# Kernel optimization log

Hardware: AMD Instinct MI355X
Metric: run time of the kernel (lower is better)

## Reference

```python
import jax, jax.numpy as jnp
import numpy as np

B, P, N, C = 8, 4, 512, 768
H = 12
HD = C // H  # 64
SCALE = HD ** -0.5


def setup_inputs() -> dict:
    key = jax.random.key(0)
    k1, k2, k3 = jax.random.split(key, 3)
    x = jax.random.normal(k1, (B, P, N, C), dtype=jnp.float32)
    W_qkv = jax.random.normal(k2, (3 * C, C), dtype=jnp.float32) * (C ** -0.5)
    W_proj = jax.random.normal(k3, (C, C), dtype=jnp.float32) * (C ** -0.5)
    b_proj = jnp.zeros((C,), dtype=jnp.float32)
    return {"x": x, "W_qkv": W_qkv, "W_proj": W_proj, "b_proj": b_proj}


def reference(x, W_qkv, W_proj, b_proj):
    b, p, n, c = x.shape
    # qkv projection (no bias): (B,P,N,3C) -> (B,P,N,3,H,HD)
    qkv = jnp.einsum('bpnc,dc->bpnd', x, W_qkv).reshape(b, p, n, 3, H, HD)
    # -> (3, B, P, H, N, HD)
    qkv = jnp.transpose(qkv, (3, 0, 1, 4, 2, 5))
    q, k, v = qkv[0], qkv[1], qkv[2]
    # scaled dot-product attention per (batch, patch, head)
    attn = jnp.einsum('bphnd,bphmd->bphnm', q * SCALE, k)
    attn = jax.nn.softmax(attn, axis=-1)
    out = jnp.einsum('bphnm,bphmd->bphnd', attn, v)
    # merge heads: (B,P,N,H,HD) -> (B,P,N,C)
    out = jnp.transpose(out, (0, 1, 3, 2, 4)).reshape(b, p, n, c)
    return jnp.einsum('bpnc,dc->bpnd', out, W_proj) + b_proj
```

## Files before the change

kernel.cpp:

```cpp
#include <hip/hip_runtime.h>

typedef _Float16 f16x8 __attribute__((ext_vector_type(8)));
typedef _Float16 f16x4 __attribute__((ext_vector_type(4)));
typedef unsigned short u16x8 __attribute__((ext_vector_type(8)));
typedef unsigned short u16x4 __attribute__((ext_vector_type(4)));
typedef float f32x4 __attribute__((ext_vector_type(4)));

#define GLOAD_LDS16(GP, LP)                                                        \
  __builtin_amdgcn_global_load_lds((const __attribute__((address_space(1))) void*)(GP), \
                                   (__attribute__((address_space(3))) void*)(LP), 16, 0, 0)

__device__ __forceinline__ unsigned int pkh(float a, float b) {
  return __builtin_bit_cast(unsigned int, __builtin_amdgcn_cvt_pkrtz(a, b));
}
__device__ __forceinline__ f16x8 ldfragh(const unsigned short* p) {
  return __builtin_bit_cast(f16x8, *(const u16x8*)p);
}
__device__ __forceinline__ f16x4 ldfragh4(const unsigned short* p) {
  return __builtin_bit_cast(f16x4, *(const u16x4*)p);
}
__device__ __forceinline__ f32x4 mfma32h(f16x8 a, f16x8 b, f32x4 c) {
  return __builtin_amdgcn_mfma_f32_16x16x32_f16(a, b, c, 0, 0, 0);
}
__device__ __forceinline__ f32x4 mfma16h(f16x4 a, f16x4 b, f32x4 c) {
  return __builtin_amdgcn_mfma_f32_16x16x16f16(a, b, c, 0, 0, 0);
}

#define MTOK   16384
#define CDIM   768
#define C3     2304
#define C2     1536
#define NX     12582912
#define NQW    1769472
#define NPW    589824

#define QSCALE_LOG2E 0.1803368801111204f

#define XB_OFF    0ul
#define WQKV_OFF  25165824ul
#define WPROJ_OFF 28704768ul
#define QK_OFF    29884416ul
#define VT_OFF    80216064ul

__global__ __launch_bounds__(256) void convert_kernel(
    const float* __restrict__ x, const float* __restrict__ wqkv,
    const float* __restrict__ wproj, unsigned short* __restrict__ xb,
    unsigned short* __restrict__ wqkvb, unsigned short* __restrict__ wprojb) {
  const int NX4 = NX / 4, NQ4 = NQW / 4, NP4 = NPW / 4;
  const int total = NX4 + NQ4 + NP4;
  for (int i = blockIdx.x * 256 + threadIdx.x; i < total; i += gridDim.x * 256) {
    const float4* src; unsigned short* dst; float scale = 1.f; int j;
    if (i < NX4) { src = (const float4*)x; dst = xb; j = i; }
    else if (i < NX4 + NQ4) {
      j = i - NX4; src = (const float4*)wqkv; dst = wqkvb;
      int d = (j * 4) / CDIM; if (d < CDIM) scale = QSCALE_LOG2E;
    } else { j = i - NX4 - NQ4; src = (const float4*)wproj; dst = wprojb; }
    float4 v = src[j];
    uint2 pk; pk.x = pkh(v.x * scale, v.y * scale); pk.y = pkh(v.z * scale, v.w * scale);
    *(uint2*)(dst + (long)j * 4) = pk;
  }
}

template <int MODE, int NCOLS>
__global__ __launch_bounds__(256) void gemm_bt(
    const unsigned short* __restrict__ A, const unsigned short* __restrict__ B,
    unsigned short* __restrict__ out_hf, unsigned short* __restrict__ out_vT,
    float* __restrict__ out_f32, const float* __restrict__ bias) {
  constexpr int K = 768;
  constexpr int NT = K / 64;
  __shared__ unsigned short As[2][128 * 64];
  __shared__ unsigned short Bs[2][128 * 64];
  const int tid = threadIdx.x;
  const int wave = tid >> 6, lane = tid & 63;
  const int wy = wave >> 1, wx = wave & 1;
  const int l15 = lane & 15, quad = lane >> 4;

  const int gid = blockIdx.x;
  const int g = gid >> 3;
  const int bm = ((g / NCOLS) << 3) + (gid & 7);
  const int bn = g % NCOLS;
  const bool swap = (MODE == 2) || (bn < 12);

  f32x4 acc[4][4];
  for (int i = 0; i < 4; i++)
    for (int j = 0; j < 4; j++) acc[i][j] = f32x4{0.f, 0.f, 0.f, 0.f};

  const unsigned short* Ab = A + (long)bm * 128 * K;
  const unsigned short* Bb = B + (long)bn * 128 * K;

  long goff[4]; int ldsoff[4];
  for (int i = 0; i < 4; i++) {
    int c = wave * 256 + i * 64 + lane;
    int row = c >> 3, q = c & 7;
    int srcq = q ^ (row & 7);
    goff[i] = (long)row * K + srcq * 8;
    ldsoff[i] = c * 8;
  }
  const int slot0 = (quad ^ (l15 & 7)) * 8;
  const int slot1 = ((4 + quad) ^ (l15 & 7)) * 8;

  for (int i = 0; i < 4; i++) {
    GLOAD_LDS16(Ab + goff[i], &As[0][ldsoff[i]]);
    GLOAD_LDS16(Bb + goff[i], &Bs[0][ldsoff[i]]);
  }

  for (int t = 0; t < NT; t++) {
    __syncthreads();
    if (t + 1 < NT) {
      const long kk = (long)(t + 1) * 64;
      const int nb = (t + 1) & 1;
      for (int i = 0; i < 4; i++) {
        GLOAD_LDS16(Ab + goff[i] + kk, &As[nb][ldsoff[i]]);
        GLOAD_LDS16(Bb + goff[i] + kk, &Bs[nb][ldsoff[i]]);
      }
    }
    const unsigned short* Ac = As[t & 1];
    const unsigned short* Bc = Bs[t & 1];
    for (int ks = 0; ks < 2; ks++) {
      const int sl = ks ? slot1 : slot0;
      f16x8 af[4], bfr[4];
      for (int mt = 0; mt < 4; mt++) af[mt]  = ldfragh(Ac + (wy * 64 + mt * 16 + l15) * 64 + sl);
      for (int nt = 0; nt < 4; nt++) bfr[nt] = ldfragh(Bc + (wx * 64 + nt * 16 + l15) * 64 + sl);
      if (swap) {
        for (int mt = 0; mt < 4; mt++)
          for (int nt = 0; nt < 4; nt++)
            acc[mt][nt] = mfma32h(bfr[nt], af[mt], acc[mt][nt]);
      } else {
        for (int mt = 0; mt < 4; mt++)
          for (int nt = 0; nt < 4; nt++)
            acc[mt][nt] = mfma32h(af[mt], bfr[nt], acc[mt][nt]);
      }
    }
  }

  if (MODE == 0) {
    if (bn < 12) {
      for (int mt = 0; mt < 4; mt++) {
        int m = bm * 128 + wy * 64 + mt * 16 + l15;
        for (int nt = 0; nt < 4; nt++) {
          int d0 = bn * 128 + wx * 64 + nt * 16 + quad * 4;
          uint2 pk; pk.x = pkh(acc[mt][nt][0], acc[mt][nt][1]);
          pk.y = pkh(acc[mt][nt][2], acc[mt][nt][3]);
          *(uint2*)(out_hf + (long)m * C2 + d0) = pk;
        }
      }
    } else {
      for (int mt = 0; mt < 4; mt++) {
        int mg = bm * 128 + wy * 64 + mt * 16 + quad * 4;
        int bp = mg >> 9, n0 = mg & 511;
        for (int nt = 0; nt < 4; nt++) {
          int dp = bn * 128 - C2 + wx * 64 + nt * 16 + l15;
          int hh = dp >> 6, e = dp & 63;
          uint2 pk; pk.x = pkh(acc[mt][nt][0], acc[mt][nt][1]);
          pk.y = pkh(acc[mt][nt][2], acc[mt][nt][3]);
          *(uint2*)(out_vT + ((long)((bp * 12 + hh) * 64 + e) * 512 + n0)) = pk;
        }
      }
    }
  } else {
    for (int nt = 0; nt < 4; nt++) {
      int d0 = bn * 128 + wx * 64 + nt * 16 + quad * 4;
      float4 bv = *(const float4*)(bias + d0);
      for (int mt = 0; mt < 4; mt++) {
        int m = bm * 128 + wy * 64 + mt * 16 + l15;
        float4 o;
        o.x = acc[mt][nt][0] + bv.x; o.y = acc[mt][nt][1] + bv.y;
        o.z = acc[mt][nt][2] + bv.z; o.w = acc[mt][nt][3] + bv.w;
        *(float4*)(out_f32 + (long)m * CDIM + d0) = o;
      }
    }
  }
}

__global__ __launch_bounds__(256, 4) void attn_kernel(
    const unsigned short* __restrict__ qk, const unsigned short* __restrict__ vT,
    unsigned short* __restrict__ aout) {
  const int bph = blockIdx.x;
  const int qt  = blockIdx.y;
  const int bp = bph / 12, h = bph % 12;
  const int tid = threadIdx.x;
  const int wave = tid >> 6, lane = tid & 63;
  const int l15 = lane & 15, quad = lane >> 4;

  __shared__ unsigned short Qs[128 * 72];
  __shared__ unsigned short Ks[64 * 72];
  __shared__ unsigned short Vs[64 * 72];

  const unsigned short* Qg = qk + (long)(bp * 512 + qt * 128) * C2 + h * 64;
  const unsigned short* Kg = qk + (long)(bp * 512) * C2 + CDIM + h * 64;
  const unsigned short* Vg = vT + (long)(bp * 12 + h) * 64 * 512;

  for (int i = 0; i < 4; i++) {
    int c = tid + i * 256;
    int row = c >> 3, c8 = c & 7;
    *(uint4*)(Qs + row * 72 + c8 * 8) = *(const uint4*)(Qg + (long)row * C2 + c8 * 8);
  }

  f32x4 o[2][4];
  float lrow[2] = {0.f, 0.f};
  for (int a = 0; a < 2; a++)
    for (int b = 0; b < 4; b++) o[a][b] = f32x4{0.f, 0.f, 0.f, 0.f};

  for (int ch = 0; ch < 8; ch++) {
    if (ch) __syncthreads();
    for (int i = 0; i < 2; i++) {
      int c = tid + i * 256;
      int row = c >> 3, c8 = c & 7;
      *(uint4*)(Ks + row * 72 + c8 * 8) = *(const uint4*)(Kg + (long)(ch * 64 + row) * C2 + c8 * 8);
      *(uint4*)(Vs + row * 72 + c8 * 8) = *(const uint4*)(Vg + (long)row * 512 + ch * 64 + c8 * 8);
    }
    __syncthreads();

    f32x4 st[2][4];
    for (int a = 0; a < 2; a++)
      for (int b = 0; b < 4; b++) st[a][b] = f32x4{0.f, 0.f, 0.f, 0.f};
    for (int ks = 0; ks < 2; ks++) {
      f16x8 qf[2];
      qf[0] = ldfragh(Qs + (wave * 32 +      l15) * 72 + ks * 32 + quad * 8);
      qf[1] = ldfragh(Qs + (wave * 32 + 16 + l15) * 72 + ks * 32 + quad * 8);
      for (int nt = 0; nt < 4; nt++) {
        f16x8 kf = ldfragh(Ks + (nt * 16 + l15) * 72 + ks * 32 + quad * 8);
        st[0][nt] = mfma32h(kf, qf[0], st[0][nt]);
        st[1][nt] = mfma32h(kf, qf[1], st[1][nt]);
      }
    }

    f16x4 pf[2][4];
    for (int mt2 = 0; mt2 < 2; mt2++) {
      float rs = 0.f;
      for (int nt = 0; nt < 4; nt++) {
        f32x4 p;
        for (int r = 0; r < 4; r++) {
          p[r] = __builtin_amdgcn_exp2f(st[mt2][nt][r]);
          rs += p[r];
        }
        uint2 pk2; pk2.x = pkh(p[0], p[1]); pk2.y = pkh(p[2], p[3]);
        pf[mt2][nt] = __builtin_bit_cast(f16x4, pk2);
      }
      lrow[mt2] += rs;
    }

    for (int nt = 0; nt < 4; nt++)
      for (int et = 0; et < 4; et++) {
        f16x4 vf = ldfragh4(Vs + (et * 16 + l15) * 72 + nt * 16 + quad * 4);
        o[0][et] = mfma16h(vf, pf[0][nt], o[0][et]);
        o[1][et] = mfma16h(vf, pf[1][nt], o[1][et]);
      }
  }

  for (int mt2 = 0; mt2 < 2; mt2++) {
    float l = lrow[mt2];
    l += __shfl_xor(l, 16);
    l += __shfl_xor(l, 32);
    float inv = 1.f / l;
    int q = qt * 128 + wave * 32 + mt2 * 16 + l15;
    for (int et = 0; et < 4; et++) {
      uint2 pk; pk.x = pkh(o[mt2][et][0] * inv, o[mt2][et][1] * inv);
      pk.y = pkh(o[mt2][et][2] * inv, o[mt2][et][3] * inv);
      *(uint2*)(aout + (long)(bp * 512 + q) * CDIM + h * 64 + et * 16 + quad * 4) = pk;
    }
  }
}

extern "C" void kernel_launch(void* const* d_in, const int* in_sizes, int n_in,
                              void* d_out, int out_size, void* d_ws, size_t ws_size,
                              hipStream_t stream) {
  (void)in_sizes; (void)n_in; (void)out_size; (void)ws_size;
  const float* x     = (const float*)d_in[0];
  const float* wqkv  = (const float*)d_in[1];
  const float* wproj = (const float*)d_in[2];
  const float* bproj = (const float*)d_in[3];
  float* out = (float*)d_out;
  char* ws = (char*)d_ws;

  unsigned short* xb     = (unsigned short*)(ws + XB_OFF);
  unsigned short* wqkvb  = (unsigned short*)(ws + WQKV_OFF);
  unsigned short* wprojb = (unsigned short*)(ws + WPROJ_OFF);
  unsigned short* qkbuf  = (unsigned short*)(ws + QK_OFF);
  unsigned short* vTbuf  = (unsigned short*)(ws + VT_OFF);
  unsigned short* attn_o = xb;

  convert_kernel<<<2048, 256, 0, stream>>>(x, wqkv, wproj, xb, wqkvb, wprojb);
  gemm_bt<0, 18><<<128 * 18, 256, 0, stream>>>(xb, wqkvb, qkbuf, vTbuf, nullptr, nullptr);
  attn_kernel<<<dim3(384, 4), 256, 0, stream>>>(qkbuf, vTbuf, attn_o);
  gemm_bt<2, 6><<<128 * 6, 256, 0, stream>>>(attn_o, wprojb, nullptr, nullptr, out, bproj);
}
```

Baseline: 268.5 us.

## Replace 128x128 GEMM with 256x256-tile, 8-wave, 4-stage pipelined GEMM

```diff
diff --git a/kernel.cpp b/kernel.cpp
--- a/kernel.cpp
+++ b/kernel.cpp
@@ -61,95 +61,130 @@
   }
 }
 
-template <int MODE, int NCOLS>
-__global__ __launch_bounds__(256) void gemm_bt(
+template <int MODE, int NTN>
+__global__ __launch_bounds__(512, 2) void gemm256(
     const unsigned short* __restrict__ A, const unsigned short* __restrict__ B,
     unsigned short* __restrict__ out_hf, unsigned short* __restrict__ out_vT,
     float* __restrict__ out_f32, const float* __restrict__ bias) {
   constexpr int K = 768;
-  constexpr int NT = K / 64;
-  __shared__ unsigned short As[2][128 * 64];
-  __shared__ unsigned short Bs[2][128 * 64];
+  constexpr int NKT = K / 32;
+  __shared__ unsigned short As[4][256 * 32];
+  __shared__ unsigned short Bs[4][256 * 32];
   const int tid = threadIdx.x;
   const int wave = tid >> 6, lane = tid & 63;
-  const int wy = wave >> 1, wx = wave & 1;
+  const int wy = wave >> 2, wx = wave & 3;
   const int l15 = lane & 15, quad = lane >> 4;
 
   const int gid = blockIdx.x;
-  const int g = gid >> 3;
-  const int bm = ((g / NCOLS) << 3) + (gid & 7);
-  const int bn = g % NCOLS;
-  const bool swap = (MODE == 2) || (bn < 12);
-
-  f32x4 acc[4][4];
-  for (int i = 0; i < 4; i++)
+  const int bn = (gid >> 3) % NTN;
+  const int bm = ((gid >> 3) / NTN) * 8 + (gid & 7);
+  const bool swap = (MODE == 2) || (bn < 6);
+
+  f32x4 acc[8][4];
+#pragma unroll
+  for (int i = 0; i < 8; i++)
+#pragma unroll
     for (int j = 0; j < 4; j++) acc[i][j] = f32x4{0.f, 0.f, 0.f, 0.f};
 
-  const unsigned short* Ab = A + (long)bm * 128 * K;
-  const unsigned short* Bb = B + (long)bn * 128 * K;
-
-  long goff[4]; int ldsoff[4];
-  for (int i = 0; i < 4; i++) {
-    int c = wave * 256 + i * 64 + lane;
-    int row = c >> 3, q = c & 7;
-    int srcq = q ^ (row & 7);
-    goff[i] = (long)row * K + srcq * 8;
-    ldsoff[i] = c * 8;
-  }
-  const int slot0 = (quad ^ (l15 & 7)) * 8;
-  const int slot1 = ((4 + quad) ^ (l15 & 7)) * 8;
-
-  for (int i = 0; i < 4; i++) {
-    GLOAD_LDS16(Ab + goff[i], &As[0][ldsoff[i]]);
-    GLOAD_LDS16(Bb + goff[i], &Bs[0][ldsoff[i]]);
-  }
-
-  for (int t = 0; t < NT; t++) {
-    __syncthreads();
-    if (t + 1 < NT) {
-      const long kk = (long)(t + 1) * 64;
-      const int nb = (t + 1) & 1;
-      for (int i = 0; i < 4; i++) {
-        GLOAD_LDS16(Ab + goff[i] + kk, &As[nb][ldsoff[i]]);
-        GLOAD_LDS16(Bb + goff[i] + kk, &Bs[nb][ldsoff[i]]);
-      }
-    }
-    const unsigned short* Ac = As[t & 1];
-    const unsigned short* Bc = Bs[t & 1];
-    for (int ks = 0; ks < 2; ks++) {
-      const int sl = ks ? slot1 : slot0;
-      f16x8 af[4], bfr[4];
-      for (int mt = 0; mt < 4; mt++) af[mt]  = ldfragh(Ac + (wy * 64 + mt * 16 + l15) * 64 + sl);
-      for (int nt = 0; nt < 4; nt++) bfr[nt] = ldfragh(Bc + (wx * 64 + nt * 16 + l15) * 64 + sl);
-      if (swap) {
-        for (int mt = 0; mt < 4; mt++)
-          for (int nt = 0; nt < 4; nt++)
-            acc[mt][nt] = mfma32h(bfr[nt], af[mt], acc[mt][nt]);
-      } else {
-        for (int mt = 0; mt < 4; mt++)
-          for (int nt = 0; nt < 4; nt++)
-            acc[mt][nt] = mfma32h(af[mt], bfr[nt], acc[mt][nt]);
-      }
-    }
-  }
+  const unsigned short* Ab = A + (long)bm * 256 * K;
+  const unsigned short* Bb = B + (long)bn * 256 * K;
+
+  const int c0 = wave * 128 + lane;
+  const int c1 = c0 + 64;
+  const int r0 = c0 >> 2, r1 = c1 >> 2;
+  const long g0 = (long)r0 * K + (long)(((c0 & 3) ^ ((r0 >> 2) & 3)) * 8);
+  const long g1 = (long)r1 * K + (long)(((c1 & 3) ^ ((r1 >> 2) & 3)) * 8);
+  const int s0 = c0 * 8, s1 = c1 * 8;
+
+#define STAGE_A(kt) { GLOAD_LDS16(Ab + g0 + (kt) * 32, &As[(kt) & 3][s0]); \
+                      GLOAD_LDS16(Ab + g1 + (kt) * 32, &As[(kt) & 3][s1]); }
+#define STAGE_B(kt) { GLOAD_LDS16(Bb + g0 + (kt) * 32, &Bs[(kt) & 3][s0]); \
+                      GLOAD_LDS16(Bb + g1 + (kt) * 32, &Bs[(kt) & 3][s1]); }
+
+  STAGE_A(0); STAGE_B(0); STAGE_A(1); STAGE_B(1); STAGE_A(2); STAGE_B(2);
+  asm volatile("s_waitcnt vmcnt(8)" ::: "memory");
+  __builtin_amdgcn_s_barrier();
+
+  const int pho = (quad ^ (l15 >> 2)) * 8;
+  const int arow = wy * 128 + l15;
+  const int brow = wx * 64 + l15;
+
+  for (int kt = 0; kt < NKT; kt++) {
+    const unsigned short* Ac = As[kt & 3];
+    const unsigned short* Bc = Bs[kt & 3];
+    f16x8 af[4], bf[4];
+#pragma unroll
+    for (int nt = 0; nt < 4; nt++) bf[nt] = ldfragh(Bc + (brow + nt * 16) * 32 + pho);
+#pragma unroll
+    for (int mt = 0; mt < 4; mt++) af[mt] = ldfragh(Ac + (arow + mt * 16) * 32 + pho);
+    if (kt < NKT - 3) STAGE_A(kt + 3);
+    __builtin_amdgcn_s_barrier();
+    asm volatile("s_waitcnt lgkmcnt(0)" ::: "memory");
+    __builtin_amdgcn_s_setprio(1);
+    if (swap) {
+#pragma unroll
+      for (int mt = 0; mt < 4; mt++)
+#pragma unroll
+        for (int nt = 0; nt < 4; nt++)
+          acc[mt][nt] = mfma32h(bf[nt], af[mt], acc[mt][nt]);
+    } else {
+#pragma unroll
+      for (int mt = 0; mt < 4; mt++)
+#pragma unroll
+        for (int nt = 0; nt < 4; nt++)
+          acc[mt][nt] = mfma32h(af[mt], bf[nt], acc[mt][nt]);
+    }
+    __builtin_amdgcn_s_setprio(0);
+    __builtin_amdgcn_s_barrier();
+#pragma unroll
+    for (int mt = 0; mt < 4; mt++) af[mt] = ldfragh(Ac + (arow + 64 + mt * 16) * 32 + pho);
+    if (kt < NKT - 3) STAGE_B(kt + 3);
+    if (kt < NKT - 3)       { asm volatile("s_waitcnt vmcnt(8)" ::: "memory"); }
+    else if (kt == NKT - 3) { asm volatile("s_waitcnt vmcnt(4)" ::: "memory"); }
+    else if (kt == NKT - 2) { asm volatile("s_waitcnt vmcnt(0)" ::: "memory"); }
+    __builtin_amdgcn_s_barrier();
+    asm volatile("s_waitcnt lgkmcnt(0)" ::: "memory");
+    __builtin_amdgcn_s_setprio(1);
+    if (swap) {
+#pragma unroll
+      for (int mt = 0; mt < 4; mt++)
+#pragma unroll
+        for (int nt = 0; nt < 4; nt++)
+          acc[4 + mt][nt] = mfma32h(bf[nt], af[mt], acc[4 + mt][nt]);
+    } else {
+#pragma unroll
+      for (int mt = 0; mt < 4; mt++)
+#pragma unroll
+        for (int nt = 0; nt < 4; nt++)
+          acc[4 + mt][nt] = mfma32h(af[mt], bf[nt], acc[4 + mt][nt]);
+    }
+    __builtin_amdgcn_s_setprio(0);
+    __builtin_amdgcn_s_barrier();
+  }
+#undef STAGE_A
+#undef STAGE_B
 
   if (MODE == 0) {
-    if (bn < 12) {
-      for (int mt = 0; mt < 4; mt++) {
-        int m = bm * 128 + wy * 64 + mt * 16 + l15;
+    if (swap) {
+#pragma unroll
+      for (int mt = 0; mt < 8; mt++) {
+        int m = bm * 256 + wy * 128 + mt * 16 + l15;
+#pragma unroll
         for (int nt = 0; nt < 4; nt++) {
-          int d0 = bn * 128 + wx * 64 + nt * 16 + quad * 4;
+          int d0 = bn * 256 + wx * 64 + nt * 16 + quad * 4;
           uint2 pk; pk.x = pkh(acc[mt][nt][0], acc[mt][nt][1]);
           pk.y = pkh(acc[mt][nt][2], acc[mt][nt][3]);
           *(uint2*)(out_hf + (long)m * C2 + d0) = pk;
         }
       }
     } else {
-      for (int mt = 0; mt < 4; mt++) {
-        int mg = bm * 128 + wy * 64 + mt * 16 + quad * 4;
+#pragma unroll
+      for (int mt = 0; mt < 8; mt++) {
+        int mg = bm * 256 + wy * 128 + mt * 16 + quad * 4;
         int bp = mg >> 9, n0 = mg & 511;
+#pragma unroll
         for (int nt = 0; nt < 4; nt++) {
-          int dp = bn * 128 - C2 + wx * 64 + nt * 16 + l15;
+          int dp = (bn - 6) * 256 + wx * 64 + nt * 16 + l15;
           int hh = dp >> 6, e = dp & 63;
           uint2 pk; pk.x = pkh(acc[mt][nt][0], acc[mt][nt][1]);
           pk.y = pkh(acc[mt][nt][2], acc[mt][nt][3]);
@@ -158,11 +193,13 @@
       }
     }
   } else {
+#pragma unroll
     for (int nt = 0; nt < 4; nt++) {
-      int d0 = bn * 128 + wx * 64 + nt * 16 + quad * 4;
+      int d0 = bn * 256 + wx * 64 + nt * 16 + quad * 4;
       float4 bv = *(const float4*)(bias + d0);
-      for (int mt = 0; mt < 4; mt++) {
-        int m = bm * 128 + wy * 64 + mt * 16 + l15;
+#pragma unroll
+      for (int mt = 0; mt < 8; mt++) {
+        int m = bm * 256 + wy * 128 + mt * 16 + l15;
         float4 o;
         o.x = acc[mt][nt][0] + bv.x; o.y = acc[mt][nt][1] + bv.y;
         o.z = acc[mt][nt][2] + bv.z; o.w = acc[mt][nt][3] + bv.w;
@@ -281,7 +318,7 @@
   unsigned short* attn_o = xb;
 
   convert_kernel<<<2048, 256, 0, stream>>>(x, wqkv, wproj, xb, wqkvb, wprojb);
-  gemm_bt<0, 18><<<128 * 18, 256, 0, stream>>>(xb, wqkvb, qkbuf, vTbuf, nullptr, nullptr);
+  gemm256<0, 9><<<576, 512, 0, stream>>>(xb, wqkvb, qkbuf, vTbuf, nullptr, nullptr);
   attn_kernel<<<dim3(384, 4), 256, 0, stream>>>(qkbuf, vTbuf, attn_o);
-  gemm_bt<2, 6><<<128 * 6, 256, 0, stream>>>(attn_o, wprojb, nullptr, nullptr, out, bproj);
-}
+  gemm256<2, 3><<<192, 512, 0, stream>>>(attn_o, wprojb, nullptr, nullptr, out, bproj);
+}
```

Result: slower. 290.3 us (+8.1%).

## Single-buffer GEMM LDS for occupancy and register-prefetch K/V tiles in attention

Applied to the files above, without the earlier changes.

```diff
diff --git a/kernel.cpp b/kernel.cpp
--- a/kernel.cpp
+++ b/kernel.cpp
@@ -62,14 +62,14 @@
 }
 
 template <int MODE, int NCOLS>
-__global__ __launch_bounds__(256) void gemm_bt(
+__global__ __launch_bounds__(256, 4) void gemm_bt(
     const unsigned short* __restrict__ A, const unsigned short* __restrict__ B,
     unsigned short* __restrict__ out_hf, unsigned short* __restrict__ out_vT,
     float* __restrict__ out_f32, const float* __restrict__ bias) {
   constexpr int K = 768;
   constexpr int NT = K / 64;
-  __shared__ unsigned short As[2][128 * 64];
-  __shared__ unsigned short Bs[2][128 * 64];
+  __shared__ unsigned short As[128 * 64];
+  __shared__ unsigned short Bs[128 * 64];
   const int tid = threadIdx.x;
   const int wave = tid >> 6, lane = tid & 63;
   const int wy = wave >> 1, wx = wave & 1;
@@ -99,28 +99,19 @@
   const int slot0 = (quad ^ (l15 & 7)) * 8;
   const int slot1 = ((4 + quad) ^ (l15 & 7)) * 8;
 
-  for (int i = 0; i < 4; i++) {
-    GLOAD_LDS16(Ab + goff[i], &As[0][ldsoff[i]]);
-    GLOAD_LDS16(Bb + goff[i], &Bs[0][ldsoff[i]]);
-  }
-
   for (int t = 0; t < NT; t++) {
     __syncthreads();
-    if (t + 1 < NT) {
-      const long kk = (long)(t + 1) * 64;
-      const int nb = (t + 1) & 1;
-      for (int i = 0; i < 4; i++) {
-        GLOAD_LDS16(Ab + goff[i] + kk, &As[nb][ldsoff[i]]);
-        GLOAD_LDS16(Bb + goff[i] + kk, &Bs[nb][ldsoff[i]]);
-      }
-    }
-    const unsigned short* Ac = As[t & 1];
-    const unsigned short* Bc = Bs[t & 1];
+    const long kk = (long)t * 64;
+    for (int i = 0; i < 4; i++) {
+      GLOAD_LDS16(Ab + goff[i] + kk, &As[ldsoff[i]]);
+      GLOAD_LDS16(Bb + goff[i] + kk, &Bs[ldsoff[i]]);
+    }
+    __syncthreads();
     for (int ks = 0; ks < 2; ks++) {
       const int sl = ks ? slot1 : slot0;
       f16x8 af[4], bfr[4];
-      for (int mt = 0; mt < 4; mt++) af[mt]  = ldfragh(Ac + (wy * 64 + mt * 16 + l15) * 64 + sl);
-      for (int nt = 0; nt < 4; nt++) bfr[nt] = ldfragh(Bc + (wx * 64 + nt * 16 + l15) * 64 + sl);
+      for (int mt = 0; mt < 4; mt++) af[mt]  = ldfragh(As + (wy * 64 + mt * 16 + l15) * 64 + sl);
+      for (int nt = 0; nt < 4; nt++) bfr[nt] = ldfragh(Bs + (wx * 64 + nt * 16 + l15) * 64 + sl);
       if (swap) {
         for (int mt = 0; mt < 4; mt++)
           for (int nt = 0; nt < 4; nt++)
@@ -190,6 +181,15 @@
   const unsigned short* Kg = qk + (long)(bp * 512) * C2 + CDIM + h * 64;
   const unsigned short* Vg = vT + (long)(bp * 12 + h) * 64 * 512;
 
+  uint4 kr[2], vr[2];
+#pragma unroll
+  for (int i = 0; i < 2; i++) {
+    int c = tid + i * 256;
+    int row = c >> 3, c8 = c & 7;
+    kr[i] = *(const uint4*)(Kg + (long)row * C2 + c8 * 8);
+    vr[i] = *(const uint4*)(Vg + (long)row * 512 + c8 * 8);
+  }
+
   for (int i = 0; i < 4; i++) {
     int c = tid + i * 256;
     int row = c >> 3, c8 = c & 7;
@@ -203,13 +203,23 @@
 
   for (int ch = 0; ch < 8; ch++) {
     if (ch) __syncthreads();
+#pragma unroll
     for (int i = 0; i < 2; i++) {
       int c = tid + i * 256;
       int row = c >> 3, c8 = c & 7;
-      *(uint4*)(Ks + row * 72 + c8 * 8) = *(const uint4*)(Kg + (long)(ch * 64 + row) * C2 + c8 * 8);
-      *(uint4*)(Vs + row * 72 + c8 * 8) = *(const uint4*)(Vg + (long)row * 512 + ch * 64 + c8 * 8);
+      *(uint4*)(Ks + row * 72 + c8 * 8) = kr[i];
+      *(uint4*)(Vs + row * 72 + c8 * 8) = vr[i];
     }
     __syncthreads();
+    if (ch < 7) {
+#pragma unroll
+      for (int i = 0; i < 2; i++) {
+        int c = tid + i * 256;
+        int row = c >> 3, c8 = c & 7;
+        kr[i] = *(const uint4*)(Kg + (long)((ch + 1) * 64 + row) * C2 + c8 * 8);
+        vr[i] = *(const uint4*)(Vg + (long)row * 512 + (ch + 1) * 64 + c8 * 8);
+      }
+    }
 
     f32x4 st[2][4];
     for (int a = 0; a < 2; a++)
```

Result: slower. 718.7 us (+167.7%).
